# Performance work log

Hardware: AMD Instinct MI355X
Metric: run time of the kernel (lower is better)

The kernel has to match this reference:

```python
import jax, jax.numpy as jnp
import numpy as np

NORM_EPS = 1e-05

def _quant_input(x):
    # per-token dynamic int8 fake-quant: s = 127 / max(|x|, 1e-5)
    s = 127.0 / jnp.clip(jnp.max(jnp.abs(x), axis=-1, keepdims=True), 1e-05, None)
    return jnp.clip(jnp.round(x * s), -128.0, 127.0) / s

def _rmsnorm(x, w, eps):
    return x * jax.lax.rsqrt(jnp.mean(x * x, axis=-1, keepdims=True) + eps) * w

def setup_inputs() -> dict:
    key = jax.random.key(0)
    k0, k1, k2 = jax.random.split(key, 3)
    dim, hidden = 2048, 5632
    x = jax.random.normal(k0, (4, 2048, dim), dtype=jnp.float32)
    w13 = jax.random.normal(k1, (2 * hidden, dim), dtype=jnp.float32) * 0.02
    w2 = jax.random.normal(k2, (dim, hidden), dtype=jnp.float32) * 0.02
    norm_w = jnp.ones((hidden,), dtype=jnp.float32)
    return {"x": x, "w13": w13, "w2": w2, "norm_w": norm_w}

def reference(x, w13, w2, norm_w):
    # BitLinear w13: quantize input, then linear
    xq = _quant_input(x)
    x13 = jnp.einsum('bsd,fd->bsf', xq, w13)  # [B,S,2H]
    x1, x3 = jnp.split(x13, 2, axis=-1)
    gated = jnp.square(jax.nn.relu(x1)) * x3  # squared-ReLU gating
    inner = _rmsnorm(gated, norm_w, NORM_EPS)
    # BitLinear w2
    iq = _quant_input(inner)
    out = jnp.einsum('bsh,dh->bsd', iq, w2)
    return out
```

## Files before the change

### kernel.cpp

```cpp
#include <hip/hip_runtime.h>

typedef unsigned short u16;
typedef __attribute__((ext_vector_type(8))) short short8;
typedef __attribute__((ext_vector_type(4))) float f32x4;
typedef __attribute__((ext_vector_type(4))) u16 ushort4v;
typedef __attribute__((ext_vector_type(8))) u16 ushort8v;

#define DIM 2048
#define HID 5632
#define F2  11264
#define TTOT 8192

#define GLD(g, l) __builtin_amdgcn_global_load_lds(                       \
    (const __attribute__((address_space(1))) void*)(g),                   \
    (__attribute__((address_space(3))) void*)(l), 16, 0, 0)

__device__ __forceinline__ u16 f2bf(float f) {
  unsigned int u = __builtin_bit_cast(unsigned int, f);
  u += 0x7FFFu + ((u >> 16) & 1u);
  return (u16)(u >> 16);
}

__global__ __launch_bounds__(256) void conv_w13(const float* __restrict__ w,
                                                u16* __restrict__ o) {
  int idx = blockIdx.x * 256 + threadIdx.x;
  int rnew = idx >> 9;
  int dc = (idx & 511) << 2;
  int b = rnew >> 5, ii = rnew & 31;
  int orig = (ii < 16) ? (b * 16 + ii) : (HID + b * 16 + (ii - 16));
  float4 v = *reinterpret_cast<const float4*>(w + (size_t)orig * DIM + dc);
  ushort4v q = {f2bf(v.x), f2bf(v.y), f2bf(v.z), f2bf(v.w)};
  *reinterpret_cast<ushort4v*>(o + (size_t)rnew * DIM + dc) = q;
}

__global__ __launch_bounds__(256) void conv_w2(const float* __restrict__ w,
                                               u16* __restrict__ o) {
  size_t e = ((size_t)blockIdx.x * 256 + threadIdx.x) * 4;
  float4 v = *reinterpret_cast<const float4*>(w + e);
  ushort4v q = {f2bf(v.x), f2bf(v.y), f2bf(v.z), f2bf(v.w)};
  *reinterpret_cast<ushort4v*>(o + e) = q;
}

__global__ __launch_bounds__(256) void quant_x(const float* __restrict__ x,
                                               u16* __restrict__ q,
                                               float* __restrict__ scale) {
  const int t = blockIdx.x;
  const float* xr = x + (size_t)t * DIM;
  const int tid = threadIdx.x;
  float4 a = *reinterpret_cast<const float4*>(xr + tid * 8);
  float4 b = *reinterpret_cast<const float4*>(xr + tid * 8 + 4);
  float v[8] = {a.x, a.y, a.z, a.w, b.x, b.y, b.z, b.w};
  float m = 0.f;
#pragma unroll
  for (int i = 0; i < 8; ++i) m = fmaxf(m, fabsf(v[i]));
#pragma unroll
  for (int off = 32; off; off >>= 1) m = fmaxf(m, __shfl_xor(m, off));
  __shared__ float red[4];
  if ((tid & 63) == 0) red[tid >> 6] = m;
  __syncthreads();
  m = fmaxf(fmaxf(red[0], red[1]), fmaxf(red[2], red[3]));
  m = fmaxf(m, 1e-5f);
  float s = 127.0f / m;
  if (tid == 0) scale[t] = m / 127.0f;
  ushort8v o;
#pragma unroll
  for (int i = 0; i < 8; ++i) {
    float r = fminf(fmaxf(rintf(v[i] * s), -128.f), 127.f);
    o[i] = f2bf(r);
  }
  *reinterpret_cast<ushort8v*>(q + (size_t)t * DIM + tid * 8) = o;
}

__global__ __launch_bounds__(256) void gate_nq(const float* __restrict__ G,
                                               const float* __restrict__ nw,
                                               u16* __restrict__ q2,
                                               float* __restrict__ s2) {
  const int t = blockIdx.x;
  const float* gr = G + (size_t)t * HID;
  const int tid = threadIdx.x;
  float4 vv[6];
  float ss = 0.f, mx = 0.f;
#pragma unroll
  for (int k = 0; k < 6; ++k) {
    int i = tid + k * 256;
    if (i < 1408) {
      float4 v = *reinterpret_cast<const float4*>(gr + i * 4);
      float4 w4 = *reinterpret_cast<const float4*>(nw + i * 4);
      vv[k] = v;
      ss += v.x * v.x + v.y * v.y + v.z * v.z + v.w * v.w;
      mx = fmaxf(mx, fmaxf(fmaxf(fabsf(v.x * w4.x), fabsf(v.y * w4.y)),
                           fmaxf(fabsf(v.z * w4.z), fabsf(v.w * w4.w))));
    }
  }
#pragma unroll
  for (int off = 32; off; off >>= 1) {
    ss += __shfl_xor(ss, off);
    mx = fmaxf(mx, __shfl_xor(mx, off));
  }
  __shared__ float rs[4], rm[4];
  if ((tid & 63) == 0) { rs[tid >> 6] = ss; rm[tid >> 6] = mx; }
  __syncthreads();
  ss = rs[0] + rs[1] + rs[2] + rs[3];
  mx = fmaxf(fmaxf(rm[0], rm[1]), fmaxf(rm[2], rm[3]));
  float rinv = 1.0f / sqrtf(ss * (1.0f / 5632.0f) + 1e-5f);
  float mi = fmaxf(mx * rinv, 1e-5f);
  float s = 127.0f / mi;
  if (tid == 0) s2[t] = mi / 127.0f;
  float fs = rinv * s;
#pragma unroll
  for (int k = 0; k < 6; ++k) {
    int i = tid + k * 256;
    if (i < 1408) {
      float4 v = vv[k];
      float4 w4 = *reinterpret_cast<const float4*>(nw + i * 4);
      ushort4v o;
      o.x = f2bf(fminf(fmaxf(rintf(v.x * w4.x * fs), -128.f), 127.f));
      o.y = f2bf(fminf(fmaxf(rintf(v.y * w4.y * fs), -128.f), 127.f));
      o.z = f2bf(fminf(fmaxf(rintf(v.z * w4.z * fs), -128.f), 127.f));
      o.w = f2bf(fminf(fmaxf(rintf(v.w * w4.w * fs), -128.f), 127.f));
      *reinterpret_cast<ushort4v*>(q2 + (size_t)t * HID + i * 4) = o;
    }
  }
}

template <int GATE, int N, int K, int Ntiles>
__global__ __launch_bounds__(512, 2) void gemm8(
    const u16* __restrict__ A, const u16* __restrict__ B,
    const float* __restrict__ rowscale, float* __restrict__ C) {
  __shared__ __attribute__((aligned(16))) u16 lds[2][2][2][256 * 32];
  constexpr int NT = K >> 6;
  const int nwg = gridDim.x;
  const int orig = blockIdx.x;
  const int qq = nwg >> 3, rr = nwg & 7, xcd = orig & 7, sidx = orig >> 3;
  const int wg = (xcd < rr ? xcd * (qq + 1) : rr * (qq + 1) + (xcd - rr) * qq) + sidx;
  const int mt = wg / Ntiles, nt = wg % Ntiles;

  const int tid = threadIdx.x;
  const int wid = tid >> 6, lane = tid & 63;
  const int wm = wid >> 2, wn = wid & 3;
  const int c16 = lane & 15, q4 = lane >> 4;
  const int rA_base = wm * 128 + c16;
  const int rB_base = wn * 64 + c16;
  const int caf = (q4 ^ ((lane >> 1) & 3)) << 3;

  const int sr = tid >> 2;
  const int scol = ((tid & 3) ^ ((tid >> 3) & 3)) << 3;
  const u16* Ar = A + ((size_t)mt * 256 + sr) * K + scol;
  const u16* Br = B + ((size_t)nt * 256 + sr) * K + scol;
  constexpr size_t rstep = (size_t)128 * K;

  f32x4 acc[8][4];
#pragma unroll
  for (int m = 0; m < 8; ++m)
#pragma unroll
    for (int n = 0; n < 4; ++n) acc[m][n] = f32x4{0.f, 0.f, 0.f, 0.f};

#define STAGE(MAT, KK, T, BUF)                                                \
  if ((T) < NT) {                                                             \
    const u16* g = ((MAT) ? Br : Ar) + (T) * 64 + (KK) * 32;                  \
    u16* l = &lds[BUF][MAT][KK][wid << 9];                                    \
    GLD(g, l);                                                                \
    GLD(g + rstep, l + 4096);                                                 \
  }
#define LDA(DB, KK, MH, AF)                                                   \
  _Pragma("unroll") for (int m = 0; m < 4; ++m)                               \
      AF[m] = *reinterpret_cast<const short8*>(                               \
          &lds[DB][0][KK][(rA_base + ((MH) * 4 + m) * 16) * 32 + caf]);
#define LDB(DB, KK, BF)                                                       \
  _Pragma("unroll") for (int n = 0; n < 4; ++n)                               \
      BF[n] = *reinterpret_cast<const short8*>(                               \
          &lds[DB][1][KK][(rB_base + n * 16) * 32 + caf]);
#define MFMA16(AF, BF, OFS)                                                   \
  __builtin_amdgcn_s_setprio(1);                                              \
  _Pragma("unroll") for (int m = 0; m < 4; ++m)                               \
      _Pragma("unroll") for (int n = 0; n < 4; ++n)                           \
          acc[(OFS) + m][n] = __builtin_amdgcn_mfma_f32_16x16x32_bf16(        \
              AF[m], BF[n], acc[(OFS) + m][n], 0, 0, 0);                      \
  __builtin_amdgcn_s_setprio(0);                                              \
  __builtin_amdgcn_sched_barrier(0);
#define BARR asm volatile("s_barrier" ::: "memory")

#define KTILE(DB, U)                                                          \
  {                                                                           \
    short8 af[4], bfr[4];                                                     \
                                    \
    LDB(DB, 0, bfr)                                                           \
    LDA(DB, 0, 0, af)                                                         \
    STAGE(0, 1, (U) + 1, DB ^ 1)                                              \
    MFMA16(af, bfr, 0)                                                        \
    BARR;                                                                     \
                                    \
    LDA(DB, 0, 1, af)                                                         \
    STAGE(1, 0, (U) + 2, DB)                                                  \
    MFMA16(af, bfr, 4)                                                        \
    BARR;                                                                     \
                                    \
    LDB(DB, 1, bfr)                                                           \
    LDA(DB, 1, 0, af)                                                         \
    STAGE(0, 0, (U) + 2, DB)                                                  \
    MFMA16(af, bfr, 0)                                                        \
    BARR;                                                                     \
               \
    LDA(DB, 1, 1, af)                                                         \
    STAGE(1, 1, (U) + 2, DB)                                                  \
    MFMA16(af, bfr, 4)                                                        \
    if ((U) + 2 < NT) asm volatile("s_waitcnt vmcnt(6)" ::: "memory");        \
    else              asm volatile("s_waitcnt vmcnt(0)" ::: "memory");        \
    BARR;                                                                     \
  }

  STAGE(1, 0, 0, 0) STAGE(0, 0, 0, 0) STAGE(1, 1, 0, 0) STAGE(0, 1, 0, 0)
  STAGE(1, 0, 1, 1) STAGE(0, 0, 1, 1) STAGE(1, 1, 1, 1)
  asm volatile("s_waitcnt vmcnt(6)" ::: "memory");
  BARR;

#pragma unroll 1
  for (int u = 0; u < NT; u += 2) {
    KTILE(0, u)
    KTILE(1, u + 1)
  }

  const int mbase0 = mt * 256 + wm * 128;
  if constexpr (GATE == 0) {
#pragma unroll
    for (int m = 0; m < 8; ++m) {
#pragma unroll
      for (int j = 0; j < 4; ++j) {
        const int row = mbase0 + m * 16 + q4 * 4 + j;
        const float sc = rowscale[row];
        float* crow = C + (size_t)row * N + nt * 256 + wn * 64 + c16;
#pragma unroll
        for (int n = 0; n < 4; ++n) crow[n * 16] = acc[m][n][j] * sc;
      }
    }
  } else {
    constexpr int H = N >> 1;
    const int gbase = (nt * 256 + wn * 64) >> 1;
#pragma unroll
    for (int m = 0; m < 8; ++m) {
#pragma unroll
      for (int j = 0; j < 4; ++j) {
        const int row = mbase0 + m * 16 + q4 * 4 + j;
        const float sc = rowscale[row];
        const float s3 = sc * sc * sc;
        float* grow = C + (size_t)row * H + gbase + c16;
#pragma unroll
        for (int p = 0; p < 2; ++p) {
          float a1 = acc[m][2 * p][j];
          float a3 = acc[m][2 * p + 1][j];
          float rl = fmaxf(a1, 0.f);
          grow[p * 16] = rl * rl * a3 * s3;
        }
      }
    }
  }
}

extern "C" void kernel_launch(void* const* d_in, const int* in_sizes, int n_in,
                              void* d_out, int out_size, void* d_ws, size_t ws_size,
                              hipStream_t stream) {
  const float* x = (const float*)d_in[0];
  const float* w13 = (const float*)d_in[1];
  const float* w2 = (const float*)d_in[2];
  const float* nw = (const float*)d_in[3];
  float* out = (float*)d_out;

  char* p = (char*)d_ws;
  u16* w13p = (u16*)p; p += (size_t)F2 * DIM * 2;
  u16* w2b = (u16*)p;  p += (size_t)DIM * HID * 2;
  u16* q2f = (u16*)p;  p += (size_t)TTOT * HID * 2;
  float* s2f = (float*)p; p += (size_t)TTOT * 4;
  const size_t fixed = (size_t)F2 * DIM * 2 + (size_t)DIM * HID * 2 +
                       (size_t)TTOT * HID * 2 + (size_t)TTOT * 4;
  const size_t perTok = (size_t)DIM * 2 + (size_t)HID * 4 + 8;
  int Tc = TTOT;
  while (Tc > 256 && fixed + (size_t)Tc * perTok > ws_size) Tc >>= 1;
  u16* q1 = (u16*)p;        p += (size_t)Tc * DIM * 2;
  float* gated = (float*)p; p += (size_t)Tc * HID * 4;
  float* s1 = (float*)p;

  conv_w13<<<F2 * DIM / 4 / 256, 256, 0, stream>>>(w13, w13p);
  conv_w2<<<DIM * HID / 4 / 256, 256, 0, stream>>>(w2, w2b);

  for (int t0 = 0; t0 < TTOT; t0 += Tc) {
    quant_x<<<Tc, 256, 0, stream>>>(x + (size_t)t0 * DIM, q1, s1);
    gemm8<1, F2, DIM, F2 / 256><<<(Tc / 256) * (F2 / 256), 512, 0, stream>>>(
        q1, w13p, s1, gated);
    gate_nq<<<Tc, 256, 0, stream>>>(gated, nw, q2f + (size_t)t0 * HID, s2f + t0);
  }
  gemm8<0, DIM, HID, DIM / 256><<<(TTOT / 256) * (DIM / 256), 512, 0, stream>>>(
      q2f, w2b, s2f, out);
}
```

Measured before the change: 597.6 us.

## Restructure GEMM k-loop into two half-phases with peeled tail iterations

Changes the main bf16 MFMA GEMM loop from four sub-phases per K tile (each issuing 16 MFMAs) to two phases that load both A halves and issue 32 MFMAs between barriers. The prefetch schedule is changed so A and B for the same k-subtile are staged together, and explicit vmcnt waits are placed at each phase. The last two iterations are peeled so the per-stage bounds check can be removed. The aim is fewer barriers, longer MFMA bursts and no branching in staging, at the cost of more live A-fragment registers and different latency hiding of global-to-LDS loads.

```diff
diff --git a/kernel.cpp b/kernel.cpp
--- a/kernel.cpp
+++ b/kernel.cpp
@@ -156,7 +156,7 @@
     for (int n = 0; n < 4; ++n) acc[m][n] = f32x4{0.f, 0.f, 0.f, 0.f};
 
 #define STAGE(MAT, KK, T, BUF)                                                \
-  if ((T) < NT) {                                                             \
+  {                                                                           \
     const u16* g = ((MAT) ? Br : Ar) + (T) * 64 + (KK) * 32;                  \
     u16* l = &lds[BUF][MAT][KK][wid << 9];                                    \
     GLD(g, l);                                                                \
@@ -170,55 +170,60 @@
   _Pragma("unroll") for (int n = 0; n < 4; ++n)                               \
       BF[n] = *reinterpret_cast<const short8*>(                               \
           &lds[DB][1][KK][(rB_base + n * 16) * 32 + caf]);
-#define MFMA16(AF, BF, OFS)                                                   \
+#define MFMA32(AF0, AF1, BF)                                                  \
   __builtin_amdgcn_s_setprio(1);                                              \
   _Pragma("unroll") for (int m = 0; m < 4; ++m)                               \
       _Pragma("unroll") for (int n = 0; n < 4; ++n)                           \
-          acc[(OFS) + m][n] = __builtin_amdgcn_mfma_f32_16x16x32_bf16(        \
-              AF[m], BF[n], acc[(OFS) + m][n], 0, 0, 0);                      \
+          acc[m][n] = __builtin_amdgcn_mfma_f32_16x16x32_bf16(                \
+              AF0[m], BF[n], acc[m][n], 0, 0, 0);                             \
+  _Pragma("unroll") for (int m = 0; m < 4; ++m)                               \
+      _Pragma("unroll") for (int n = 0; n < 4; ++n)                           \
+          acc[4 + m][n] = __builtin_amdgcn_mfma_f32_16x16x32_bf16(            \
+              AF1[m], BF[n], acc[4 + m][n], 0, 0, 0);                         \
   __builtin_amdgcn_s_setprio(0);                                              \
   __builtin_amdgcn_sched_barrier(0);
 #define BARR asm volatile("s_barrier" ::: "memory")
-
-#define KTILE(DB, U)                                                          \
+#define VMC(NN) asm volatile("s_waitcnt vmcnt(" #NN ")" ::: "memory")
+
+#define KT2(DB, U, STGA, VMA, STGB, VMB)                                      \
   {                                                                           \
-    short8 af[4], bfr[4];                                                     \
-                                    \
+    short8 bfr[4], af0[4], af1[4];                                            \
+                                                            \
     LDB(DB, 0, bfr)                                                           \
-    LDA(DB, 0, 0, af)                                                         \
-    STAGE(0, 1, (U) + 1, DB ^ 1)                                              \
-    MFMA16(af, bfr, 0)                                                        \
+    LDA(DB, 0, 0, af0)                                                        \
+    LDA(DB, 0, 1, af1)                                                        \
+    if (STGA) {                                                               \
+      STAGE(0, 1, (U) + 1, (DB) ^ 1)                                          \
+      STAGE(1, 1, (U) + 1, (DB) ^ 1)                                          \
+    }                                                                         \
+    MFMA32(af0, af1, bfr)                                                     \
+    VMC(VMA);                                                                 \
     BARR;                                                                     \
-                                    \
-    LDA(DB, 0, 1, af)                                                         \
-    STAGE(1, 0, (U) + 2, DB)                                                  \
-    MFMA16(af, bfr, 4)                                                        \
+                                                            \
+    LDB(DB, 1, bfr)                                                           \
+    LDA(DB, 1, 0, af0)                                                        \
+    LDA(DB, 1, 1, af1)                                                        \
+    if (STGB) {                                                               \
+      STAGE(0, 0, (U) + 2, DB)                                                \
+      STAGE(1, 0, (U) + 2, DB)                                                \
+    }                                                                         \
+    MFMA32(af0, af1, bfr)                                                     \
+    VMC(VMB);                                                                 \
     BARR;                                                                     \
-                                    \
-    LDB(DB, 1, bfr)                                                           \
-    LDA(DB, 1, 0, af)                                                         \
-    STAGE(0, 0, (U) + 2, DB)                                                  \
-    MFMA16(af, bfr, 0)                                                        \
-    BARR;                                                                     \
-               \
-    LDA(DB, 1, 1, af)                                                         \
-    STAGE(1, 1, (U) + 2, DB)                                                  \
-    MFMA16(af, bfr, 4)                                                        \
-    if ((U) + 2 < NT) asm volatile("s_waitcnt vmcnt(6)" ::: "memory");        \
-    else              asm volatile("s_waitcnt vmcnt(0)" ::: "memory");        \
-    BARR;                                                                     \
   }
 
   STAGE(1, 0, 0, 0) STAGE(0, 0, 0, 0) STAGE(1, 1, 0, 0) STAGE(0, 1, 0, 0)
-  STAGE(1, 0, 1, 1) STAGE(0, 0, 1, 1) STAGE(1, 1, 1, 1)
-  asm volatile("s_waitcnt vmcnt(6)" ::: "memory");
+  STAGE(1, 0, 1, 1) STAGE(0, 0, 1, 1)
+  VMC(4);
   BARR;
 
 #pragma unroll 1
-  for (int u = 0; u < NT; u += 2) {
-    KTILE(0, u)
-    KTILE(1, u + 1)
-  }
+  for (int u = 0; u < NT - 2; u += 2) {
+    KT2(0, u, 1, 8, 1, 8)
+    KT2(1, u + 1, 1, 8, 1, 8)
+  }
+  KT2(0, NT - 2, 1, 8, 0, 8)
+  KT2(1, NT - 1, 0, 0, 0, 0)
 
   const int mbase0 = mt * 256 + wm * 128;
   if constexpr (GATE == 0) {
```

Result: no change. 604.3 us (+1.1%).

## Shrink GEMM tile to 128x256 with BK=32 and simple double buffering

Applied to the files above, without the earlier changes.

Reduces the GEMM block tile from 256x256 to 128x256 rows and halves the K step to 32, replacing the deep multi-stage async-load pipeline with a simple two-buffer scheme that waits for all loads each step. LDS and accumulator registers shrink, and launch bounds request four blocks per CU for more occupancy and a larger grid. In exchange, each step now fully drains outstanding memory loads, the priority hints are removed, and operand reuse per tile drops.

```diff
diff --git a/kernel.cpp b/kernel.cpp
--- a/kernel.cpp
+++ b/kernel.cpp
@@ -124,11 +124,11 @@
 }
 
 template <int GATE, int N, int K, int Ntiles>
-__global__ __launch_bounds__(512, 2) void gemm8(
+__global__ __launch_bounds__(512, 4) void gemm8(
     const u16* __restrict__ A, const u16* __restrict__ B,
     const float* __restrict__ rowscale, float* __restrict__ C) {
-  __shared__ __attribute__((aligned(16))) u16 lds[2][2][2][256 * 32];
-  constexpr int NT = K >> 6;
+  __shared__ __attribute__((aligned(16))) u16 lds[2][384 * 32];
+  constexpr int NT = K >> 5;
   const int nwg = gridDim.x;
   const int orig = blockIdx.x;
   const int qq = nwg >> 3, rr = nwg & 7, xcd = orig & 7, sidx = orig >> 3;
@@ -139,79 +139,60 @@
   const int wid = tid >> 6, lane = tid & 63;
   const int wm = wid >> 2, wn = wid & 3;
   const int c16 = lane & 15, q4 = lane >> 4;
-  const int rA_base = wm * 128 + c16;
+  const int rA_base = wm * 64 + c16;
   const int rB_base = wn * 64 + c16;
   const int caf = (q4 ^ ((lane >> 1) & 3)) << 3;
 
   const int sr = tid >> 2;
   const int scol = ((tid & 3) ^ ((tid >> 3) & 3)) << 3;
-  const u16* Ar = A + ((size_t)mt * 256 + sr) * K + scol;
+  const u16* Ar = A + ((size_t)mt * 128 + sr) * K + scol;
   const u16* Br = B + ((size_t)nt * 256 + sr) * K + scol;
-  constexpr size_t rstep = (size_t)128 * K;
-
-  f32x4 acc[8][4];
-#pragma unroll
-  for (int m = 0; m < 8; ++m)
+
+  f32x4 acc[4][4];
+#pragma unroll
+  for (int m = 0; m < 4; ++m)
 #pragma unroll
     for (int n = 0; n < 4; ++n) acc[m][n] = f32x4{0.f, 0.f, 0.f, 0.f};
 
-#define STAGE(MAT, KK, T, BUF)                                                \
-  if ((T) < NT) {                                                             \
-    const u16* g = ((MAT) ? Br : Ar) + (T) * 64 + (KK) * 32;                  \
-    u16* l = &lds[BUF][MAT][KK][wid << 9];                                    \
-    GLD(g, l);                                                                \
-    GLD(g + rstep, l + 4096);                                                 \
-  }
-#define LDA(DB, KK, MH, AF)                                                   \
+#define STAGE(T, BUF)                                                         \
+  {                                                                           \
+    const u16* ga = Ar + (T) * 32;                                            \
+    const u16* gb = Br + (T) * 32;                                            \
+    u16* la = &lds[BUF][wid << 9];                                            \
+    u16* lb = &lds[BUF][4096 + (wid << 9)];                                   \
+    GLD(ga, la);                                                              \
+    GLD(gb, lb);                                                              \
+    GLD(gb + (size_t)128 * K, lb + 4096);                                     \
+  }
+#define LDA(BUF, AF)                                                          \
   _Pragma("unroll") for (int m = 0; m < 4; ++m)                               \
       AF[m] = *reinterpret_cast<const short8*>(                               \
-          &lds[DB][0][KK][(rA_base + ((MH) * 4 + m) * 16) * 32 + caf]);
-#define LDB(DB, KK, BF)                                                       \
+          &lds[BUF][(rA_base + m * 16) * 32 + caf]);
+#define LDB(BUF, BF)                                                          \
   _Pragma("unroll") for (int n = 0; n < 4; ++n)                               \
       BF[n] = *reinterpret_cast<const short8*>(                               \
-          &lds[DB][1][KK][(rB_base + n * 16) * 32 + caf]);
-#define MFMA16(AF, BF, OFS)                                                   \
-  __builtin_amdgcn_s_setprio(1);                                              \
+          &lds[BUF][4096 + (rB_base + n * 16) * 32 + caf]);
+#define MFMA16(AF, BF)                                                        \
   _Pragma("unroll") for (int m = 0; m < 4; ++m)                               \
       _Pragma("unroll") for (int n = 0; n < 4; ++n)                           \
-          acc[(OFS) + m][n] = __builtin_amdgcn_mfma_f32_16x16x32_bf16(        \
-              AF[m], BF[n], acc[(OFS) + m][n], 0, 0, 0);                      \
-  __builtin_amdgcn_s_setprio(0);                                              \
-  __builtin_amdgcn_sched_barrier(0);
+          acc[m][n] = __builtin_amdgcn_mfma_f32_16x16x32_bf16(                \
+              AF[m], BF[n], acc[m][n], 0, 0, 0);
 #define BARR asm volatile("s_barrier" ::: "memory")
-
-#define KTILE(DB, U)                                                          \
+#define VMC0 asm volatile("s_waitcnt vmcnt(0)" ::: "memory")
+
+#define KTILE(BUF, U)                                                         \
   {                                                                           \
     short8 af[4], bfr[4];                                                     \
-                                    \
-    LDB(DB, 0, bfr)                                                           \
-    LDA(DB, 0, 0, af)                                                         \
-    STAGE(0, 1, (U) + 1, DB ^ 1)                                              \
-    MFMA16(af, bfr, 0)                                                        \
+    LDB(BUF, bfr)                                                             \
+    LDA(BUF, af)                                                              \
+    if ((U) + 1 < NT) STAGE((U) + 1, (BUF) ^ 1)                               \
+    MFMA16(af, bfr)                                                           \
+    VMC0;                                                                     \
     BARR;                                                                     \
-                                    \
-    LDA(DB, 0, 1, af)                                                         \
-    STAGE(1, 0, (U) + 2, DB)                                                  \
-    MFMA16(af, bfr, 4)                                                        \
-    BARR;                                                                     \
-                                    \
-    LDB(DB, 1, bfr)                                                           \
-    LDA(DB, 1, 0, af)                                                         \
-    STAGE(0, 0, (U) + 2, DB)                                                  \
-    MFMA16(af, bfr, 0)                                                        \
-    BARR;                                                                     \
-               \
-    LDA(DB, 1, 1, af)                                                         \
-    STAGE(1, 1, (U) + 2, DB)                                                  \
-    MFMA16(af, bfr, 4)                                                        \
-    if ((U) + 2 < NT) asm volatile("s_waitcnt vmcnt(6)" ::: "memory");        \
-    else              asm volatile("s_waitcnt vmcnt(0)" ::: "memory");        \
-    BARR;                                                                     \
-  }
-
-  STAGE(1, 0, 0, 0) STAGE(0, 0, 0, 0) STAGE(1, 1, 0, 0) STAGE(0, 1, 0, 0)
-  STAGE(1, 0, 1, 1) STAGE(0, 0, 1, 1) STAGE(1, 1, 1, 1)
-  asm volatile("s_waitcnt vmcnt(6)" ::: "memory");
+  }
+
+  STAGE(0, 0)
+  VMC0;
   BARR;
 
 #pragma unroll 1
@@ -220,10 +201,10 @@
     KTILE(1, u + 1)
   }
 
-  const int mbase0 = mt * 256 + wm * 128;
+  const int mbase0 = mt * 128 + wm * 64;
   if constexpr (GATE == 0) {
 #pragma unroll
-    for (int m = 0; m < 8; ++m) {
+    for (int m = 0; m < 4; ++m) {
 #pragma unroll
       for (int j = 0; j < 4; ++j) {
         const int row = mbase0 + m * 16 + q4 * 4 + j;
@@ -237,7 +218,7 @@
     constexpr int H = N >> 1;
     const int gbase = (nt * 256 + wn * 64) >> 1;
 #pragma unroll
-    for (int m = 0; m < 8; ++m) {
+    for (int m = 0; m < 4; ++m) {
 #pragma unroll
       for (int j = 0; j < 4; ++j) {
         const int row = mbase0 + m * 16 + q4 * 4 + j;
@@ -284,10 +265,10 @@
 
   for (int t0 = 0; t0 < TTOT; t0 += Tc) {
     quant_x<<<Tc, 256, 0, stream>>>(x + (size_t)t0 * DIM, q1, s1);
-    gemm8<1, F2, DIM, F2 / 256><<<(Tc / 256) * (F2 / 256), 512, 0, stream>>>(
+    gemm8<1, F2, DIM, F2 / 256><<<(Tc / 128) * (F2 / 256), 512, 0, stream>>>(
         q1, w13p, s1, gated);
     gate_nq<<<Tc, 256, 0, stream>>>(gated, nw, q2f + (size_t)t0 * HID, s2f + t0);
   }
-  gemm8<0, DIM, HID, DIM / 256><<<(TTOT / 256) * (DIM / 256), 512, 0, stream>>>(
+  gemm8<0, DIM, HID, DIM / 256><<<(TTOT / 128) * (DIM / 256), 512, 0, stream>>>(
       q2f, w2b, s2f, out);
 }
```

New measurement: 747.8 us. +25.1%, slower.
